# Performance work log

Measured on AMD Instinct MI355X. Metric: run time of the kernel, lower is better.

## Reference

```python
import jax, jax.numpy as jnp
import numpy as np

N, E = 50000, 800000          # nodes, edges
IN, OUT, ED = 128, 64, 32     # in_dim, out_dim, edge_dim


def setup_inputs() -> dict:
    key = jax.random.key(0)
    ks = jax.random.split(key, 8)
    init = lambda k, shape, fan: jax.random.normal(k, shape, jnp.float32) * np.float32(1.0 / np.sqrt(fan))
    return {
        "x": jax.random.normal(ks[0], (N, IN), jnp.float32),
        "edge_attr": jax.random.normal(ks[1], (E, ED), jnp.float32),
        "edge_index": jax.random.randint(ks[2], (2, E), 0, N),
        "W_fc": init(ks[3], (IN, OUT), IN),
        "b_fc": jnp.zeros((OUT,), jnp.float32),
        "W_attn": init(ks[4], (2 * OUT + ED, 1), 2 * OUT + ED),
        "b_attn": jnp.zeros((1,), jnp.float32),
        "W_edge": init(ks[5], (ED, OUT), ED),
        "b_edge": jnp.zeros((OUT,), jnp.float32),
        "W_self": init(ks[6], (IN, OUT), IN),
        "b_self": jnp.zeros((OUT,), jnp.float32),
    }


def reference(x, edge_attr, edge_index, W_fc, b_fc, W_attn, b_attn,
              W_edge, b_edge, W_self, b_self):
    row, col = edge_index[0], edge_index[1]   # src, dst node ids per edge
    # node transform: z = fc(x)  (batch norm disabled -> identity)
    z = x @ W_fc + b_fc                        # [N, OUT]
    # edge-dependent attention logits: cat(z_src, z_dst, ex) -> scalar
    z2 = jnp.concatenate([z[row], z[col], edge_attr], axis=1)   # [E, 2*OUT+ED]
    e = jax.nn.leaky_relu(z2 @ W_attn + b_attn, negative_slope=0.2)  # [E, 1]
    # edge feature transform for aggregation
    ez = edge_attr @ W_edge + b_edge           # [E, OUT]
    # segment softmax over incoming edges of each destination node
    m = jax.ops.segment_max(e, col, num_segments=N)   # [N, 1]
    m = jnp.where(jnp.isfinite(m), m, 0.0)             # nodes with no in-edges
    p = jnp.exp(e - m[col])                             # [E, 1]
    denom = jax.ops.segment_sum(p, col, num_segments=N)
    alpha = p / jnp.maximum(denom[col], 1e-16)          # [E, 1]
    # attention-weighted aggregation of node messages + edge messages
    h = jax.ops.segment_sum(alpha * (z[row] + ez), col, num_segments=N)  # [N, OUT]
    # self-loop residual with its own transform
    h = h + (x @ W_self + b_self)
    return h
```

## Files before the change

kernel.cpp:

```cpp
#include <hip/hip_runtime.h>

typedef unsigned int uint;
typedef unsigned short u16;

#define IN_DIM 128
#define OUT_DIM 64
#define ED_DIM 32
#define WT_STRIDE 136
#define CAP 64

typedef __bf16 bf16x8 __attribute__((ext_vector_type(8)));
typedef float f32x4 __attribute__((ext_vector_type(4)));

static __device__ __forceinline__ float bf2f(u16 u) {
    return __uint_as_float(((uint)u) << 16);
}
static __device__ __forceinline__ u16 f2bf(float f) {
    uint u = __float_as_uint(f);
    uint r = u + 0x7fffu + ((u >> 16) & 1u);
    return (u16)(r >> 16);
}
static __device__ __forceinline__ float ldf(const void* p, size_t i, bool f32m) {
    return f32m ? ((const float*)p)[i] : bf2f(((const u16*)p)[i]);
}

__global__ __launch_bounds__(256) void k0_prep(
    const u16* __restrict__ xraw, const void* __restrict__ Wfc,
    const void* __restrict__ Wself, u16* __restrict__ Wt_fc,
    u16* __restrict__ Wt_s, uint* __restrict__ flag)
{
    __shared__ int cnt;
    if (threadIdx.x == 0) cnt = 0;
    __syncthreads();
    float v = bf2f(xraw[threadIdx.x]);
    if (!(fabsf(v) <= 64.f)) atomicAdd(&cnt, 1);
    __syncthreads();
    bool f32m = cnt > 0;
    if (threadIdx.x == 0) flag[0] = f32m ? 1u : 0u;
    for (int i = threadIdx.x; i < IN_DIM * OUT_DIM; i += 256) {
        int k = i >> 6, n = i & 63;
        u16 vf = f32m ? f2bf(((const float*)Wfc)[i]) : ((const u16*)Wfc)[i];
        u16 vs = f32m ? f2bf(((const float*)Wself)[i]) : ((const u16*)Wself)[i];
        Wt_fc[(size_t)n * WT_STRIDE + k] = vf;
        Wt_s [(size_t)n * WT_STRIDE + k] = vs;
    }
}

__global__ __launch_bounds__(256) void k1_mfma(
    const void* __restrict__ x, const u16* __restrict__ Wt_fc,
    const u16* __restrict__ Wt_s, const void* __restrict__ bfc,
    const void* __restrict__ Wattn, const void* __restrict__ bself,
    u16* __restrict__ z_bf, float* __restrict__ hself,
    float* __restrict__ a_src, float* __restrict__ a_dst,
    uint* __restrict__ cursor, const uint* __restrict__ flag, int n_nodes)
{
    bool f32m = flag[0] != 0u;
    int tid = blockIdx.x * 256 + threadIdx.x;
    int stride = gridDim.x * 256;
    for (int i = tid; i < n_nodes; i += stride) cursor[i] = 0u;

    int wave = threadIdx.x >> 6, lane = threadIdx.x & 63;
    int q = lane >> 4, c = lane & 15;
    int nb = blockIdx.x * 64 + wave * 16;
    if (nb >= n_nodes) return;

    bf16x8 Bfc[4][4], Bs[4][4];
    #pragma unroll
    for (int kt = 0; kt < 4; kt++)
        #pragma unroll
        for (int nt = 0; nt < 4; nt++) {
            size_t off = (size_t)(nt * 16 + c) * WT_STRIDE + kt * 32 + q * 8;
            Bfc[kt][nt] = *(const bf16x8*)(Wt_fc + off);
            Bs [kt][nt] = *(const bf16x8*)(Wt_s + off);
        }

    f32x4 az[4], as_[4];
    #pragma unroll
    for (int nt = 0; nt < 4; nt++) {
        az[nt]  = (f32x4){0.f, 0.f, 0.f, 0.f};
        as_[nt] = (f32x4){0.f, 0.f, 0.f, 0.f};
    }

    int m = nb + c; if (m >= n_nodes) m = n_nodes - 1;

    #pragma unroll
    for (int kt = 0; kt < 4; kt++) {
        int k0 = kt * 32 + q * 8;
        bf16x8 a;
        if (f32m) {
            const float* xr = (const float*)x + (size_t)m * IN_DIM + k0;
            float4 f0 = *(const float4*)xr;
            float4 f1 = *(const float4*)(xr + 4);
            a[0] = (__bf16)f0.x; a[1] = (__bf16)f0.y; a[2] = (__bf16)f0.z; a[3] = (__bf16)f0.w;
            a[4] = (__bf16)f1.x; a[5] = (__bf16)f1.y; a[6] = (__bf16)f1.z; a[7] = (__bf16)f1.w;
        } else {
            a = *(const bf16x8*)((const u16*)x + (size_t)m * IN_DIM + k0);
        }
        #pragma unroll
        for (int nt = 0; nt < 4; nt++) {
            az[nt]  = __builtin_amdgcn_mfma_f32_16x16x32_bf16(a, Bfc[kt][nt], az[nt], 0, 0, 0);
            as_[nt] = __builtin_amdgcn_mfma_f32_16x16x32_bf16(a, Bs[kt][nt], as_[nt], 0, 0, 0);
        }
    }

    float was[4], wad[4], bz[4], bs[4];
    #pragma unroll
    for (int nt = 0; nt < 4; nt++) {
        was[nt] = ldf(Wattn, nt * 16 + c, f32m);
        wad[nt] = ldf(Wattn, 64 + nt * 16 + c, f32m);
        bz[nt]  = ldf(bfc, nt * 16 + c, f32m);
        bs[nt]  = ldf(bself, nt * 16 + c, f32m);
    }
    #pragma unroll
    for (int reg = 0; reg < 4; reg++) {
        int nn = nb + q * 4 + reg;
        bool ok = nn < n_nodes;
        float ps = 0.f, pd = 0.f;
        #pragma unroll
        for (int nt = 0; nt < 4; nt++) {
            float zv = az[nt][reg] + bz[nt];
            float hv = as_[nt][reg] + bs[nt];
            float zp = __shfl_xor(zv, 1, 64);
            if (ok) {
                hself[(size_t)nn * OUT_DIM + nt * 16 + c] = hv;
                if (!(c & 1)) {
                    uint u = (uint)f2bf(zv) | ((uint)f2bf(zp) << 16);
                    *(uint*)(z_bf + (size_t)nn * OUT_DIM + nt * 16 + c) = u;
                }
            }
            ps = fmaf(zv, was[nt], ps);
            pd = fmaf(zv, wad[nt], pd);
        }
        #pragma unroll
        for (int off = 8; off; off >>= 1) {
            ps += __shfl_xor(ps, off, 64);
            pd += __shfl_xor(pd, off, 64);
        }
        if (ok && c == 0) { a_src[nn] = ps; a_dst[nn] = pd; }
    }
}

__global__ __launch_bounds__(256) void k4_scatter(
    const int* __restrict__ ei, const void* __restrict__ edge_attr,
    const void* __restrict__ Wattn, const void* __restrict__ battn,
    const float* __restrict__ a_src, const float* __restrict__ a_dst,
    uint* __restrict__ cursor, uint4* __restrict__ meta,
    u16* __restrict__ ea_bf, const uint* __restrict__ flag,
    int use_ea, int n_edges)
{
    bool f32m = flag[0] != 0u;
    int e = blockIdx.x * 256 + threadIdx.x;
    if (e >= n_edges) return;
    int r = ei[e];
    int c = ei[n_edges + e];
    float s = a_src[r] + a_dst[c] + ldf(battn, 0, f32m);

    uint wpk[16];
    if (f32m) {
        const float* ea = (const float*)edge_attr + (size_t)e * ED_DIM;
        const float* wa = (const float*)Wattn + 128;
        #pragma unroll
        for (int j = 0; j < 16; j++) {
            float v0 = ea[2 * j], v1 = ea[2 * j + 1];
            s = fmaf(v0, wa[2 * j], fmaf(v1, wa[2 * j + 1], s));
            wpk[j] = (uint)f2bf(v0) | ((uint)f2bf(v1) << 16);
        }
    } else {
        const uint* ea = (const uint*)((const u16*)edge_attr + (size_t)e * ED_DIM);
        const u16* wa = (const u16*)Wattn + 128;
        #pragma unroll
        for (int j = 0; j < 16; j++) {
            uint u = ea[j];
            s = fmaf(__uint_as_float(u << 16), bf2f(wa[2 * j]),
                fmaf(__uint_as_float(u & 0xffff0000u), bf2f(wa[2 * j + 1]), s));
            wpk[j] = u;
        }
    }
    float l = s > 0.f ? s : 0.2f * s;
    float p = __expf(l);
    uint pos = atomicAdd(&cursor[c], 1u);
    if (pos < CAP)
        meta[((size_t)c << 6) + pos] = make_uint4((uint)r, (uint)e, __float_as_uint(p), 0u);
    if (use_ea) {
        uint4* dst = (uint4*)(ea_bf + (size_t)e * ED_DIM);
        dst[0] = make_uint4(wpk[0], wpk[1], wpk[2], wpk[3]);
        dst[1] = make_uint4(wpk[4], wpk[5], wpk[6], wpk[7]);
        dst[2] = make_uint4(wpk[8], wpk[9], wpk[10], wpk[11]);
        dst[3] = make_uint4(wpk[12], wpk[13], wpk[14], wpk[15]);
    }
}

__global__ __launch_bounds__(256) void k5_agg(
    const void* __restrict__ edge_attr, const void* __restrict__ Wedge,
    const void* __restrict__ bedge, const u16* __restrict__ z_bf,
    const float* __restrict__ hself, const uint* __restrict__ cursor,
    const uint4* __restrict__ meta, const u16* __restrict__ ea_bf,
    void* __restrict__ out, const uint* __restrict__ flag,
    int use_ea, int n_nodes)
{
    bool f32m = flag[0] != 0u;
    __shared__ float sWedge[ED_DIM * OUT_DIM];
    for (int i = threadIdx.x; i < ED_DIM * OUT_DIM; i += 256)
        sWedge[i] = ldf(Wedge, i, f32m);
    __syncthreads();

    int lane = threadIdx.x & 63;
    int n = (blockIdx.x * 256 + threadIdx.x) >> 6;
    if (n >= n_nodes) return;

    uint deg = cursor[n];
    if (deg > CAP) deg = CAP;
    float h = hself[(size_t)n * OUT_DIM + lane];

    if (deg > 0) {
        const uint4* seg = meta + ((size_t)n << 6);
        int l32 = lane & 31;
        bool hi = lane >= 32;
        float d = 0.f, accz = 0.f, accea = 0.f;
        for (uint i = 0; i < deg; i += 2) {
            uint i1 = (i + 1 < deg) ? i + 1 : i;
            uint4 m0 = seg[i];
            uint4 m1 = seg[i1];
            float p0 = __uint_as_float(m0.z);
            float p1 = (i + 1 < deg) ? __uint_as_float(m1.z) : 0.f;
            float z0 = bf2f(z_bf[(size_t)m0.x * OUT_DIM + lane]);
            float z1 = bf2f(z_bf[(size_t)m1.x * OUT_DIM + lane]);
            d += p0 + p1;
            accz = fmaf(p0, z0, fmaf(p1, z1, accz));
            uint eid = hi ? m1.y : m0.y;
            float pe = hi ? p1 : p0;
            float eav = use_ea
                ? bf2f(ea_bf[(size_t)eid * ED_DIM + l32])
                : ldf(edge_attr, (size_t)eid * ED_DIM + l32, f32m);
            accea = fmaf(pe, eav, accea);
        }
        accea += __shfl_xor(accea, 32, 64);

        float inv = 1.f / fmaxf(d, 1e-30f);
        float hea = accea * inv;
        float he = ldf(bedge, lane, f32m);
        #pragma unroll 8
        for (int j = 0; j < ED_DIM; j++) {
            float hj = __shfl(hea, j, 64);
            he = fmaf(hj, sWedge[j * OUT_DIM + lane], he);
        }
        h += accz * inv + he;
    }

    size_t oi = (size_t)n * OUT_DIM + lane;
    if (f32m) ((float*)out)[oi] = h;
    else      ((u16*)out)[oi] = f2bf(h);
}

extern "C" void kernel_launch(void* const* d_in, const int* in_sizes, int n_in,
                              void* d_out, int out_size, void* d_ws, size_t ws_size,
                              hipStream_t stream) {
    const void* x         = d_in[0];
    const void* edge_attr = d_in[1];
    const int*  ei        = (const int*)d_in[2];
    const void* Wfc       = d_in[3];
    const void* bfc       = d_in[4];
    const void* Wattn     = d_in[5];
    const void* battn     = d_in[6];
    const void* Wedge     = d_in[7];
    const void* bedge     = d_in[8];
    const void* Wself     = d_in[9];
    const void* bself     = d_in[10];

    const int N = in_sizes[0] / IN_DIM;
    const int E = in_sizes[1] / ED_DIM;

    char* ws = (char*)d_ws;
    size_t off = 0;
    auto alloc = [&](size_t bytes) -> void* {
        void* p = ws + off;
        off += (bytes + 255) & ~(size_t)255;
        return p;
    };
    u16*   z_bf   = (u16*)  alloc((size_t)N * OUT_DIM * sizeof(u16));
    float* hself  = (float*)alloc((size_t)N * OUT_DIM * sizeof(float));
    float* a_src  = (float*)alloc((size_t)N * sizeof(float));
    float* a_dst  = (float*)alloc((size_t)N * sizeof(float));
    uint*  cursor = (uint*) alloc((size_t)N * sizeof(uint));
    uint4* meta   = (uint4*)alloc((size_t)N * CAP * sizeof(uint4));
    u16*   Wt_fc  = (u16*)  alloc((size_t)OUT_DIM * WT_STRIDE * sizeof(u16));
    u16*   Wt_s   = (u16*)  alloc((size_t)OUT_DIM * WT_STRIDE * sizeof(u16));
    uint*  flag   = (uint*) alloc(256);

    size_t ea_bytes = (size_t)E * ED_DIM * sizeof(u16);
    int use_ea = (off + ea_bytes + 4096 <= ws_size) ? 1 : 0;
    u16* ea_bf = use_ea ? (u16*)alloc(ea_bytes) : (u16*)ws;

    int mfmaBlocks = (N + 63) / 64;
    int nodeBlocks = (N + 3) / 4;
    int edgeBlocks = (E + 255) / 256;

    k0_prep<<<1, 256, 0, stream>>>((const u16*)x, Wfc, Wself, Wt_fc, Wt_s, flag);
    k1_mfma<<<mfmaBlocks, 256, 0, stream>>>(x, Wt_fc, Wt_s, bfc, Wattn, bself,
                                            z_bf, hself, a_src, a_dst,
                                            cursor, flag, N);
    k4_scatter<<<edgeBlocks, 256, 0, stream>>>(ei, edge_attr, Wattn, battn,
                                               a_src, a_dst, cursor,
                                               meta, ea_bf, flag, use_ea, E);
    k5_agg<<<nodeBlocks, 256, 0, stream>>>(edge_attr, Wedge, bedge, z_bf, hself,
                                           cursor, meta, ea_bf, d_out, flag,
                                           use_ea, N);
}
```

Measured before the change: 361.5 us.

## Move attention logit computation into aggregation and shrink scatter to edge ids

The scatter kernel now only records edge ids into per-destination slots, replacing 16-byte metadata records and dropping the bf16 copy of edge_attr. The aggregation kernel recomputes each edge's attention logit from a_src, a_dst and a warp-shuffle dot product of edge_attr with W_attn, and also gathers the source id from edge_index. This removes a full write and reread of edge features and metadata, at the cost of extra gathers (edge_index, a_src) and reading fp32 edge_attr in the aggregation loop.

```diff
diff --git a/kernel.cpp b/kernel.cpp
--- a/kernel.cpp
+++ b/kernel.cpp
@@ -140,63 +140,26 @@
     }
 }
 
-__global__ __launch_bounds__(256) void k4_scatter(
+__global__ __launch_bounds__(256) void k4_slot(
+    const int* __restrict__ ei, uint* __restrict__ cursor,
+    uint* __restrict__ seid, int n_edges)
+{
+    int e = blockIdx.x * 256 + threadIdx.x;
+    if (e >= n_edges) return;
+    int c = ei[n_edges + e];
+    uint pos = atomicAdd(&cursor[c], 1u);
+    if (pos < CAP) seid[((size_t)c << 6) + pos] = (uint)e;
+}
+
+__global__ __launch_bounds__(256) void k5_agg(
     const int* __restrict__ ei, const void* __restrict__ edge_attr,
     const void* __restrict__ Wattn, const void* __restrict__ battn,
+    const void* __restrict__ Wedge, const void* __restrict__ bedge,
+    const u16* __restrict__ z_bf, const float* __restrict__ hself,
     const float* __restrict__ a_src, const float* __restrict__ a_dst,
-    uint* __restrict__ cursor, uint4* __restrict__ meta,
-    u16* __restrict__ ea_bf, const uint* __restrict__ flag,
-    int use_ea, int n_edges)
-{
-    bool f32m = flag[0] != 0u;
-    int e = blockIdx.x * 256 + threadIdx.x;
-    if (e >= n_edges) return;
-    int r = ei[e];
-    int c = ei[n_edges + e];
-    float s = a_src[r] + a_dst[c] + ldf(battn, 0, f32m);
-
-    uint wpk[16];
-    if (f32m) {
-        const float* ea = (const float*)edge_attr + (size_t)e * ED_DIM;
-        const float* wa = (const float*)Wattn + 128;
-        #pragma unroll
-        for (int j = 0; j < 16; j++) {
-            float v0 = ea[2 * j], v1 = ea[2 * j + 1];
-            s = fmaf(v0, wa[2 * j], fmaf(v1, wa[2 * j + 1], s));
-            wpk[j] = (uint)f2bf(v0) | ((uint)f2bf(v1) << 16);
-        }
-    } else {
-        const uint* ea = (const uint*)((const u16*)edge_attr + (size_t)e * ED_DIM);
-        const u16* wa = (const u16*)Wattn + 128;
-        #pragma unroll
-        for (int j = 0; j < 16; j++) {
-            uint u = ea[j];
-            s = fmaf(__uint_as_float(u << 16), bf2f(wa[2 * j]),
-                fmaf(__uint_as_float(u & 0xffff0000u), bf2f(wa[2 * j + 1]), s));
-            wpk[j] = u;
-        }
-    }
-    float l = s > 0.f ? s : 0.2f * s;
-    float p = __expf(l);
-    uint pos = atomicAdd(&cursor[c], 1u);
-    if (pos < CAP)
-        meta[((size_t)c << 6) + pos] = make_uint4((uint)r, (uint)e, __float_as_uint(p), 0u);
-    if (use_ea) {
-        uint4* dst = (uint4*)(ea_bf + (size_t)e * ED_DIM);
-        dst[0] = make_uint4(wpk[0], wpk[1], wpk[2], wpk[3]);
-        dst[1] = make_uint4(wpk[4], wpk[5], wpk[6], wpk[7]);
-        dst[2] = make_uint4(wpk[8], wpk[9], wpk[10], wpk[11]);
-        dst[3] = make_uint4(wpk[12], wpk[13], wpk[14], wpk[15]);
-    }
-}
-
-__global__ __launch_bounds__(256) void k5_agg(
-    const void* __restrict__ edge_attr, const void* __restrict__ Wedge,
-    const void* __restrict__ bedge, const u16* __restrict__ z_bf,
-    const float* __restrict__ hself, const uint* __restrict__ cursor,
-    const uint4* __restrict__ meta, const u16* __restrict__ ea_bf,
+    const uint* __restrict__ cursor, const uint* __restrict__ seid,
     void* __restrict__ out, const uint* __restrict__ flag,
-    int use_ea, int n_nodes)
+    int n_edges, int n_nodes)
 {
     bool f32m = flag[0] != 0u;
     __shared__ float sWedge[ED_DIM * OUT_DIM];
@@ -213,26 +176,39 @@
     float h = hself[(size_t)n * OUT_DIM + lane];
 
     if (deg > 0) {
-        const uint4* seg = meta + ((size_t)n << 6);
         int l32 = lane & 31;
         bool hi = lane >= 32;
+        float wa_l = ldf(Wattn, 128 + l32, f32m);
+        float bat = ldf(battn, 0, f32m);
+        float adst = a_dst[n];
+        const uint* seg = seid + ((size_t)n << 6);
+
         float d = 0.f, accz = 0.f, accea = 0.f;
         for (uint i = 0; i < deg; i += 2) {
-            uint i1 = (i + 1 < deg) ? i + 1 : i;
-            uint4 m0 = seg[i];
-            uint4 m1 = seg[i1];
-            float p0 = __uint_as_float(m0.z);
-            float p1 = (i + 1 < deg) ? __uint_as_float(m1.z) : 0.f;
-            float z0 = bf2f(z_bf[(size_t)m0.x * OUT_DIM + lane]);
-            float z1 = bf2f(z_bf[(size_t)m1.x * OUT_DIM + lane]);
+            bool v1 = (i + 1 < deg);
+            uint j1 = v1 ? i + 1 : i;
+            uint e0 = seg[i];
+            uint e1 = seg[j1];
+            uint r0 = (uint)ei[e0];
+            uint r1 = (uint)ei[e1];
+            uint myE = hi ? e1 : e0;
+            uint myR = hi ? r1 : r0;
+            float eav = ldf(edge_attr, (size_t)myE * ED_DIM + l32, f32m);
+            float t = eav * wa_l;
+            #pragma unroll
+            for (int off = 16; off; off >>= 1) t += __shfl_xor(t, off, 64);
+            float s = a_src[myR] + adst + t + bat;
+            float l_ = s > 0.f ? s : 0.2f * s;
+            float p = __expf(l_);
+            if (hi && !v1) p = 0.f;
+            float po = __shfl_xor(p, 32, 64);
+            float p0 = hi ? po : p;
+            float p1 = hi ? p : po;
+            float z0 = bf2f(z_bf[(size_t)r0 * OUT_DIM + lane]);
+            float z1 = bf2f(z_bf[(size_t)r1 * OUT_DIM + lane]);
             d += p0 + p1;
             accz = fmaf(p0, z0, fmaf(p1, z1, accz));
-            uint eid = hi ? m1.y : m0.y;
-            float pe = hi ? p1 : p0;
-            float eav = use_ea
-                ? bf2f(ea_bf[(size_t)eid * ED_DIM + l32])
-                : ldf(edge_attr, (size_t)eid * ED_DIM + l32, f32m);
-            accea = fmaf(pe, eav, accea);
+            accea = fmaf(p, eav, accea);
         }
         accea += __shfl_xor(accea, 32, 64);
 
@@ -282,14 +258,10 @@
     float* a_src  = (float*)alloc((size_t)N * sizeof(float));
     float* a_dst  = (float*)alloc((size_t)N * sizeof(float));
     uint*  cursor = (uint*) alloc((size_t)N * sizeof(uint));
-    uint4* meta   = (uint4*)alloc((size_t)N * CAP * sizeof(uint4));
+    uint*  seid   = (uint*) alloc((size_t)N * CAP * sizeof(uint));
     u16*   Wt_fc  = (u16*)  alloc((size_t)OUT_DIM * WT_STRIDE * sizeof(u16));
     u16*   Wt_s   = (u16*)  alloc((size_t)OUT_DIM * WT_STRIDE * sizeof(u16));
     uint*  flag   = (uint*) alloc(256);
-
-    size_t ea_bytes = (size_t)E * ED_DIM * sizeof(u16);
-    int use_ea = (off + ea_bytes + 4096 <= ws_size) ? 1 : 0;
-    u16* ea_bf = use_ea ? (u16*)alloc(ea_bytes) : (u16*)ws;
 
     int mfmaBlocks = (N + 63) / 64;
     int nodeBlocks = (N + 3) / 4;
@@ -299,10 +271,9 @@
     k1_mfma<<<mfmaBlocks, 256, 0, stream>>>(x, Wt_fc, Wt_s, bfc, Wattn, bself,
                                             z_bf, hself, a_src, a_dst,
                                             cursor, flag, N);
-    k4_scatter<<<edgeBlocks, 256, 0, stream>>>(ei, edge_attr, Wattn, battn,
-                                               a_src, a_dst, cursor,
-                                               meta, ea_bf, flag, use_ea, E);
-    k5_agg<<<nodeBlocks, 256, 0, stream>>>(edge_attr, Wedge, bedge, z_bf, hself,
-                                           cursor, meta, ea_bf, d_out, flag,
-                                           use_ea, N);
-}
+    k4_slot<<<edgeBlocks, 256, 0, stream>>>(ei, cursor, seid, E);
+    k5_agg<<<nodeBlocks, 256, 0, stream>>>(ei, edge_attr, Wattn, battn,
+                                           Wedge, bedge, z_bf, hself,
+                                           a_src, a_dst, cursor, seid,
+                                           d_out, flag, E, N);
+}
```

Result: slower. 396.7 us (+9.7%).

## Shrink edge metadata to uint2, unroll aggregation by four, pre-swizzle MFMA weights

Applied to the files above, without the earlier changes.

Per-edge metadata now holds only (edge id, p) in 8 bytes instead of 16, and the aggregation kernel recovers the source node from edge_index. The aggregation loop handles four edges per iteration: each half-wave loads two metadata entries and shares source ids and weights with a cross-half shuffle, giving more independent gathers in flight. Weights for the node transform are pre-arranged into MFMA fragment order, so each fragment is loaded contiguously inside the k-loop instead of being held in registers up front. The cost is an extra dependent gather from edge_index per edge, and the weights are now re-read from memory on every iteration.

```diff
diff --git a/kernel.cpp b/kernel.cpp
--- a/kernel.cpp
+++ b/kernel.cpp
@@ -6,7 +6,6 @@
 #define IN_DIM 128
 #define OUT_DIM 64
 #define ED_DIM 32
-#define WT_STRIDE 136
 #define CAP 64
 
 typedef __bf16 bf16x8 __attribute__((ext_vector_type(8)));
@@ -38,11 +37,14 @@
     bool f32m = cnt > 0;
     if (threadIdx.x == 0) flag[0] = f32m ? 1u : 0u;
     for (int i = threadIdx.x; i < IN_DIM * OUT_DIM; i += 256) {
-        int k = i >> 6, n = i & 63;
-        u16 vf = f32m ? f2bf(((const float*)Wfc)[i]) : ((const u16*)Wfc)[i];
-        u16 vs = f32m ? f2bf(((const float*)Wself)[i]) : ((const u16*)Wself)[i];
-        Wt_fc[(size_t)n * WT_STRIDE + k] = vf;
-        Wt_s [(size_t)n * WT_STRIDE + k] = vs;
+        int j = i & 7, lane = (i >> 3) & 63, frag = i >> 9;
+        int kt = frag >> 2, nt = frag & 3;
+        int q = lane >> 4, c = lane & 15;
+        int k = kt * 32 + q * 8 + j;
+        int n = nt * 16 + c;
+        int src = k * OUT_DIM + n;
+        Wt_fc[i] = f32m ? f2bf(((const float*)Wfc)[src]) : ((const u16*)Wfc)[src];
+        Wt_s [i] = f32m ? f2bf(((const float*)Wself)[src]) : ((const u16*)Wself)[src];
     }
 }
 
@@ -64,16 +66,6 @@
     int nb = blockIdx.x * 64 + wave * 16;
     if (nb >= n_nodes) return;
 
-    bf16x8 Bfc[4][4], Bs[4][4];
-    #pragma unroll
-    for (int kt = 0; kt < 4; kt++)
-        #pragma unroll
-        for (int nt = 0; nt < 4; nt++) {
-            size_t off = (size_t)(nt * 16 + c) * WT_STRIDE + kt * 32 + q * 8;
-            Bfc[kt][nt] = *(const bf16x8*)(Wt_fc + off);
-            Bs [kt][nt] = *(const bf16x8*)(Wt_s + off);
-        }
-
     f32x4 az[4], as_[4];
     #pragma unroll
     for (int nt = 0; nt < 4; nt++) {
@@ -98,8 +90,11 @@
         }
         #pragma unroll
         for (int nt = 0; nt < 4; nt++) {
-            az[nt]  = __builtin_amdgcn_mfma_f32_16x16x32_bf16(a, Bfc[kt][nt], az[nt], 0, 0, 0);
-            as_[nt] = __builtin_amdgcn_mfma_f32_16x16x32_bf16(a, Bs[kt][nt], as_[nt], 0, 0, 0);
+            int fo = ((kt * 4 + nt) * 64 + lane) * 8;
+            bf16x8 bf = *(const bf16x8*)(Wt_fc + fo);
+            bf16x8 bs = *(const bf16x8*)(Wt_s + fo);
+            az[nt]  = __builtin_amdgcn_mfma_f32_16x16x32_bf16(a, bf, az[nt], 0, 0, 0);
+            as_[nt] = __builtin_amdgcn_mfma_f32_16x16x32_bf16(a, bs, as_[nt], 0, 0, 0);
         }
     }
 
@@ -144,7 +139,7 @@
     const int* __restrict__ ei, const void* __restrict__ edge_attr,
     const void* __restrict__ Wattn, const void* __restrict__ battn,
     const float* __restrict__ a_src, const float* __restrict__ a_dst,
-    uint* __restrict__ cursor, uint4* __restrict__ meta,
+    uint* __restrict__ cursor, uint2* __restrict__ meta,
     u16* __restrict__ ea_bf, const uint* __restrict__ flag,
     int use_ea, int n_edges)
 {
@@ -180,7 +175,7 @@
     float p = __expf(l);
     uint pos = atomicAdd(&cursor[c], 1u);
     if (pos < CAP)
-        meta[((size_t)c << 6) + pos] = make_uint4((uint)r, (uint)e, __float_as_uint(p), 0u);
+        meta[((size_t)c << 6) + pos] = make_uint2((uint)e, __float_as_uint(p));
     if (use_ea) {
         uint4* dst = (uint4*)(ea_bf + (size_t)e * ED_DIM);
         dst[0] = make_uint4(wpk[0], wpk[1], wpk[2], wpk[3]);
@@ -191,12 +186,12 @@
 }
 
 __global__ __launch_bounds__(256) void k5_agg(
-    const void* __restrict__ edge_attr, const void* __restrict__ Wedge,
-    const void* __restrict__ bedge, const u16* __restrict__ z_bf,
-    const float* __restrict__ hself, const uint* __restrict__ cursor,
-    const uint4* __restrict__ meta, const u16* __restrict__ ea_bf,
-    void* __restrict__ out, const uint* __restrict__ flag,
-    int use_ea, int n_nodes)
+    const int* __restrict__ ei, const void* __restrict__ edge_attr,
+    const void* __restrict__ Wedge, const void* __restrict__ bedge,
+    const u16* __restrict__ z_bf, const float* __restrict__ hself,
+    const uint* __restrict__ cursor, const uint2* __restrict__ meta,
+    const u16* __restrict__ ea_bf, void* __restrict__ out,
+    const uint* __restrict__ flag, int use_ea, int n_nodes)
 {
     bool f32m = flag[0] != 0u;
     __shared__ float sWedge[ED_DIM * OUT_DIM];
@@ -213,26 +208,43 @@
     float h = hself[(size_t)n * OUT_DIM + lane];
 
     if (deg > 0) {
-        const uint4* seg = meta + ((size_t)n << 6);
         int l32 = lane & 31;
         bool hi = lane >= 32;
+        const uint2* seg = meta + ((size_t)n << 6);
         float d = 0.f, accz = 0.f, accea = 0.f;
-        for (uint i = 0; i < deg; i += 2) {
-            uint i1 = (i + 1 < deg) ? i + 1 : i;
-            uint4 m0 = seg[i];
-            uint4 m1 = seg[i1];
-            float p0 = __uint_as_float(m0.z);
-            float p1 = (i + 1 < deg) ? __uint_as_float(m1.z) : 0.f;
-            float z0 = bf2f(z_bf[(size_t)m0.x * OUT_DIM + lane]);
-            float z1 = bf2f(z_bf[(size_t)m1.x * OUT_DIM + lane]);
-            d += p0 + p1;
-            accz = fmaf(p0, z0, fmaf(p1, z1, accz));
-            uint eid = hi ? m1.y : m0.y;
-            float pe = hi ? p1 : p0;
-            float eav = use_ea
-                ? bf2f(ea_bf[(size_t)eid * ED_DIM + l32])
-                : ldf(edge_attr, (size_t)eid * ED_DIM + l32, f32m);
-            accea = fmaf(pe, eav, accea);
+
+        for (uint i = 0; i < deg; i += 4) {
+            uint j1 = (i + 1 < deg) ? i + 1 : i;
+            uint j2 = (i + 2 < deg) ? i + 2 : i;
+            uint j3 = (i + 3 < deg) ? i + 3 : j2;
+            bool vA = hi ? (i + 1 < deg) : true;
+            bool vB = hi ? (i + 3 < deg) : (i + 2 < deg);
+            uint2 mA = seg[hi ? j1 : i];
+            uint2 mB = seg[hi ? j3 : j2];
+            float pA = vA ? __uint_as_float(mA.y) : 0.f;
+            float pB = vB ? __uint_as_float(mB.y) : 0.f;
+            uint rA = (uint)ei[mA.x];
+            uint rB = (uint)ei[mB.x];
+            float eavA = use_ea ? bf2f(ea_bf[(size_t)mA.x * ED_DIM + l32])
+                                : ldf(edge_attr, (size_t)mA.x * ED_DIM + l32, f32m);
+            float eavB = use_ea ? bf2f(ea_bf[(size_t)mB.x * ED_DIM + l32])
+                                : ldf(edge_attr, (size_t)mB.x * ED_DIM + l32, f32m);
+            accea = fmaf(pA, eavA, fmaf(pB, eavB, accea));
+
+            float pAo = __shfl_xor(pA, 32, 64);
+            float pBo = __shfl_xor(pB, 32, 64);
+            uint  rAo = __shfl_xor(rA, 32, 64);
+            uint  rBo = __shfl_xor(rB, 32, 64);
+            float p0 = hi ? pAo : pA, p1 = hi ? pA : pAo;
+            float p2 = hi ? pBo : pB, p3 = hi ? pB : pBo;
+            uint  r0 = hi ? rAo : rA, r1 = hi ? rA : rAo;
+            uint  r2 = hi ? rBo : rB, r3 = hi ? rB : rBo;
+            float z0 = bf2f(z_bf[(size_t)r0 * OUT_DIM + lane]);
+            float z1 = bf2f(z_bf[(size_t)r1 * OUT_DIM + lane]);
+            float z2 = bf2f(z_bf[(size_t)r2 * OUT_DIM + lane]);
+            float z3 = bf2f(z_bf[(size_t)r3 * OUT_DIM + lane]);
+            d += (p0 + p1) + (p2 + p3);
+            accz = fmaf(p0, z0, fmaf(p1, z1, fmaf(p2, z2, fmaf(p3, z3, accz))));
         }
         accea += __shfl_xor(accea, 32, 64);
 
@@ -282,9 +294,9 @@
     float* a_src  = (float*)alloc((size_t)N * sizeof(float));
     float* a_dst  = (float*)alloc((size_t)N * sizeof(float));
     uint*  cursor = (uint*) alloc((size_t)N * sizeof(uint));
-    uint4* meta   = (uint4*)alloc((size_t)N * CAP * sizeof(uint4));
-    u16*   Wt_fc  = (u16*)  alloc((size_t)OUT_DIM * WT_STRIDE * sizeof(u16));
-    u16*   Wt_s   = (u16*)  alloc((size_t)OUT_DIM * WT_STRIDE * sizeof(u16));
+    uint2* meta   = (uint2*)alloc((size_t)N * CAP * sizeof(uint2));
+    u16*   Wt_fc  = (u16*)  alloc((size_t)IN_DIM * OUT_DIM * sizeof(u16));
+    u16*   Wt_s   = (u16*)  alloc((size_t)IN_DIM * OUT_DIM * sizeof(u16));
     uint*  flag   = (uint*) alloc(256);
 
     size_t ea_bytes = (size_t)E * ED_DIM * sizeof(u16);
@@ -302,7 +314,7 @@
     k4_scatter<<<edgeBlocks, 256, 0, stream>>>(ei, edge_attr, Wattn, battn,
                                                a_src, a_dst, cursor,
                                                meta, ea_bf, flag, use_ea, E);
-    k5_agg<<<nodeBlocks, 256, 0, stream>>>(edge_attr, Wedge, bedge, z_bf, hself,
-                                           cursor, meta, ea_bf, d_out, flag,
-                                           use_ea, N);
-}
+    k5_agg<<<nodeBlocks, 256, 0, stream>>>(ei, edge_attr, Wedge, bedge,
+                                           z_bf, hself, cursor, meta, ea_bf,
+                                           d_out, flag, use_ea, N);
+}
```

Result: faster. 345.5 us (-4.4%).
